# Performance work log

Measured on AMD Instinct MI355X. Metric: run time of the kernel, lower is better.

The kernel has to match this reference:

```python
import jax, jax.numpy as jnp
from jax import lax
import numpy as np

INPUT_DIM = 64
AUX_DIM = 32
HIDDEN = [512, 512]
OUTPUT_DIM = 128
BATCH = 64
SEQ = 512


def _lstm_params(key, in_dim, hidden):
    # PyTorch nn.LSTM init: U(-1/sqrt(H), 1/sqrt(H)); gate order i,f,g,o
    k = 1.0 / np.sqrt(hidden)
    ks = jax.random.split(key, 4)
    W_ih = jax.random.uniform(ks[0], (4 * hidden, in_dim), jnp.float32, -k, k)
    W_hh = jax.random.uniform(ks[1], (4 * hidden, hidden), jnp.float32, -k, k)
    b_ih = jax.random.uniform(ks[2], (4 * hidden,), jnp.float32, -k, k)
    b_hh = jax.random.uniform(ks[3], (4 * hidden,), jnp.float32, -k, k)
    return W_ih, W_hh, b_ih, b_hh


def setup_inputs() -> dict:
    key = jax.random.key(0)
    k_x, k_aux, k_l0, k_l1, k_w, k_b = jax.random.split(key, 6)
    primary_input = jax.random.normal(k_x, (BATCH, SEQ, INPUT_DIM), jnp.float32)
    auxiliary_input = jax.random.normal(k_aux, (BATCH, AUX_DIM), jnp.float32)
    W_ih0, W_hh0, b_ih0, b_hh0 = _lstm_params(k_l0, INPUT_DIM + AUX_DIM, HIDDEN[0])
    W_ih1, W_hh1, b_ih1, b_hh1 = _lstm_params(k_l1, HIDDEN[0], HIDDEN[1])
    k_out = 1.0 / np.sqrt(HIDDEN[-1])
    W_out = jax.random.uniform(k_w, (OUTPUT_DIM, HIDDEN[-1]), jnp.float32, -k_out, k_out)
    b_out = jax.random.uniform(k_b, (OUTPUT_DIM,), jnp.float32, -k_out, k_out)
    return {
        "primary_input": primary_input, "auxiliary_input": auxiliary_input,
        "W_ih0": W_ih0, "W_hh0": W_hh0, "b_ih0": b_ih0, "b_hh0": b_hh0,
        "W_ih1": W_ih1, "W_hh1": W_hh1, "b_ih1": b_ih1, "b_hh1": b_hh1,
        "W_out": W_out, "b_out": b_out,
    }


def _lstm_layer(x, W_ih, W_hh, b_ih, b_hh):
    # x: [B, S, D] -> hidden sequence [B, S, H]; zero initial (h, c)
    B = x.shape[0]
    H = W_hh.shape[1]
    # Precompute input projection for all timesteps: [B, S, 4H]
    x_proj = jnp.einsum('bsd,gd->bsg', x, W_ih) + b_ih + b_hh

    def step(carry, xt):
        h, c = carry  # [B, H] each
        gates = xt + h @ W_hh.T  # [B, 4H]
        i, f, g, o = jnp.split(gates, 4, axis=-1)
        i = jax.nn.sigmoid(i)
        f = jax.nn.sigmoid(f)
        g = jnp.tanh(g)
        o = jax.nn.sigmoid(o)
        c = f * c + i * g
        h = o * jnp.tanh(c)
        return (h, c), h

    h0 = jnp.zeros((B, H), x.dtype)
    (_, _), hs = lax.scan(step, (h0, h0), jnp.swapaxes(x_proj, 0, 1))
    return jnp.swapaxes(hs, 0, 1)  # [B, S, H]


def reference(primary_input, auxiliary_input,
              W_ih0, W_hh0, b_ih0, b_hh0,
              W_ih1, W_hh1, b_ih1, b_hh1,
              W_out, b_out):
    S = primary_input.shape[1]
    aux = jnp.broadcast_to(auxiliary_input[:, None, :],
                           (auxiliary_input.shape[0], S, auxiliary_input.shape[1]))
    x = jnp.concatenate([primary_input, aux], axis=2)  # [B, S, input+aux]
    x = _lstm_layer(x, W_ih0, W_hh0, b_ih0, b_hh0)
    x = _lstm_layer(x, W_ih1, W_hh1, b_ih1, b_hh1)
    last = x[:, -1, :]  # [B, H]
    return last @ W_out.T + b_out  # [B, output_dim]
```

## Files before the change

### kernel.cpp

```cpp
#include <hip/hip_runtime.h>

#define BATCH 64
#define SEQ   512
#define HID   512
#define DPRIM 64
#define DAUX  32
#define DIN   96
#define CT    16
#define NCHUNK 32
#define NBAT  32
#define WP    520
#define XPI   104
#define PST   33

#define WS_HB0HI  0u
#define WS_HB0LO  131072u
#define WS_HB1HI  262144u
#define WS_HB1LO  393216u
#define WS_SLOT0  524288u
#define WS_SLOT1  526336u
#define WS_GDONE  528384u
#define WS_XPD    530432u
#define WS_STATE_END 532480u
#define WS_PHH0HI 532480u
#define WS_PHH0LO 2629632u
#define WS_PHH1HI 4726784u
#define WS_PHH1LO 6823936u
#define WS_PIH1HI 8921088u
#define WS_PIH1LO 11018240u
#define WS_PIH0HI 13115392u
#define WS_PIH0LO 13508608u
#define WS_BSUM0  13901824u
#define WS_BSUM1  13910016u
#define WS_WOT    13918208u
#define WS_HIST   14180352u
#define WS_XP0    18374656u
#define WS_XP1    26763264u

typedef short s16x8 __attribute__((ext_vector_type(8)));
typedef float f32x4 __attribute__((ext_vector_type(4)));
typedef unsigned long long u64x2 __attribute__((ext_vector_type(2)));
typedef unsigned long long u64t;
typedef unsigned int u32t;
typedef unsigned short u16t;

__device__ __forceinline__ float sigm(float x)  { return 1.f / (1.f + __expf(-x)); }
__device__ __forceinline__ float tanh_f(float x){ return 1.f - 2.f / (__expf(2.f * x) + 1.f); }
__device__ __forceinline__ u16t f2b(float f) {
    u32t u = __float_as_uint(f);
    u += 0x7fffu + ((u >> 16) & 1u);
    return (u16t)(u >> 16);
}
__device__ __forceinline__ void split2(float f, u16t* hi, u16t* lo) {
    u16t h = f2b(f);
    float r = f - __uint_as_float((u32t)h << 16);
    *hi = h; *lo = f2b(r);
}
__device__ __forceinline__ u64t ld_coh64(const u64t* p) {
    return __hip_atomic_load(p, __ATOMIC_RELAXED, __HIP_MEMORY_SCOPE_AGENT);
}
__device__ __forceinline__ void st_coh64w(u64t* p, u64t v) {
    __hip_atomic_store(p, v, __ATOMIC_RELAXED, __HIP_MEMORY_SCOPE_AGENT);
}
__device__ __forceinline__ void st_cohf(float* p, float v) {
    __hip_atomic_store(p, v, __ATOMIC_RELAXED, __HIP_MEMORY_SCOPE_AGENT);
}
__device__ __forceinline__ int ld_slot(const int* p) {
    return __hip_atomic_load(p, __ATOMIC_RELAXED, __HIP_MEMORY_SCOPE_AGENT);
}
__device__ __forceinline__ void st_slot(int* p, int v) {
    __hip_atomic_store(p, v, __ATOMIC_RELAXED, __HIP_MEMORY_SCOPE_AGENT);
}
#define MFMA16(a,b,c) __builtin_amdgcn_mfma_f32_16x16x32_bf16(a,b,c,0,0,0)

__device__ __forceinline__ void load_afrag(const u16t* ph, const u16t* pl,
                                           int u0, int col, int kg, int rt, int kh,
                                           s16x8* ah, s16x8* al) {
    int r = rt * 16 + col;
    int grow = (r >> 3) * HID + u0 + (r & 7);
    const u16t* sh = ph + (size_t)grow * HID;
    const u16t* sl = pl + (size_t)grow * HID;
#pragma unroll
    for (int k2 = 0; k2 < 8; ++k2) {
        int ko = (kh * 8 + k2) * 32 + kg * 8;
        ah[k2] = *(const s16x8*)(sh + ko);
        al[k2] = *(const s16x8*)(sl + ko);
    }
}

__global__ void prep_kernel(const float* __restrict__ Wih0, const float* __restrict__ Whh0,
                            const float* __restrict__ bih0, const float* __restrict__ bhh0,
                            const float* __restrict__ Wih1, const float* __restrict__ Whh1,
                            const float* __restrict__ bih1, const float* __restrict__ bhh1,
                            const float* __restrict__ Wout, char* __restrict__ ws)
{
    int idx = blockIdx.x * 256 + threadIdx.x;
    u16t h, l;
    split2(Whh0[idx], &h, &l);
    ((u16t*)(ws + WS_PHH0HI))[idx] = h; ((u16t*)(ws + WS_PHH0LO))[idx] = l;
    split2(Whh1[idx], &h, &l);
    ((u16t*)(ws + WS_PHH1HI))[idx] = h; ((u16t*)(ws + WS_PHH1LO))[idx] = l;
    split2(Wih1[idx], &h, &l);
    ((u16t*)(ws + WS_PIH1HI))[idx] = h; ((u16t*)(ws + WS_PIH1LO))[idx] = l;
    if (idx < 2048 * 96) {
        split2(Wih0[idx], &h, &l);
        ((u16t*)(ws + WS_PIH0HI))[idx] = h; ((u16t*)(ws + WS_PIH0LO))[idx] = l;
    }
    if (idx < 2048) {
        ((float*)(ws + WS_BSUM0))[idx] = bih0[idx] + bhh0[idx];
        ((float*)(ws + WS_BSUM1))[idx] = bih1[idx] + bhh1[idx];
    }
    if (idx < 65536) {
        ((float*)(ws + WS_WOT))[idx] = Wout[(size_t)(idx & 127) * HID + (idx >> 7)];
    }
}

__device__ __forceinline__ void do_step(
    int t, int c, int tl, int tid, int col, int kg,
    int rt, int bt, int kh,
    int b0, int u0, int ug,
    const s16x8* ahf, const s16x8* alf,
    u16t* Hti, u16t* Htl, float* Ps, float* Cs,
    u16t* hbhi, u16t* hblo, int* slots_self,
    const float* xp_self, bool coh_xq, u32t* hist_ring)
{
    const int p = t & 1;
    float4 xq = {0.f, 0.f, 0.f, 0.f};
    if (tid < 256) {
        int b = tid >> 3, u = tid & 7;
        const float* xr = xp_self + (size_t)(b * CT + tl) * 32 + u * 4;
        if (coh_xq) {
            u64t w0 = ld_coh64((const u64t*)xr);
            u64t w1 = ld_coh64((const u64t*)xr + 1);
            xq.x = __uint_as_float((u32t)w0); xq.y = __uint_as_float((u32t)(w0 >> 32));
            xq.z = __uint_as_float((u32t)w1); xq.w = __uint_as_float((u32t)(w1 >> 32));
        } else {
            xq = *(const float4*)xr;
        }
    }
    if (tid < 64) {
        const int* sp = slots_self + tid * 4;
        while (true) {
            int v = ld_slot(sp);
            if (__all(v >= t)) break;
            __builtin_amdgcn_s_sleep(2);
        }
    }
    __syncthreads();
    asm volatile("" ::: "memory");
    {
        int bl  = tid & 31;
        int bk0 = tid >> 5;
        const u64t* gh = (const u64t*)hbhi;
        const u64t* gl = (const u64t*)hblo;
#pragma unroll
        for (int q = 0; q < 4; ++q) {
            int block = bk0 + q * 16;
            size_t tg = (((size_t)(p ^ 1) * 64 + block) * 64 + b0 + bl) * 2;
            u64t h0 = ld_coh64(gh + tg);
            u64t h1 = ld_coh64(gh + tg + 1);
            u64t l0 = ld_coh64(gl + tg);
            u64t l1 = ld_coh64(gl + tg + 1);
            int lt = (block * 32 + bl) * 8;
            *(u64x2*)(Hti + lt) = (u64x2){h0, h1};
            *(u64x2*)(Htl + lt) = (u64x2){l0, l1};
        }
    }
    __syncthreads();
    {
        f32x4 a0 = {0.f, 0.f, 0.f, 0.f}, a1 = {0.f, 0.f, 0.f, 0.f};
#pragma unroll
        for (int k2 = 0; k2 < 8; ++k2) {
            int blk = kh * 32 + k2 * 4 + kg;
            const u16t* hb = Hti + ((size_t)blk * 32 + bt * 16 + col) * 8;
            const u16t* lb = Htl + ((size_t)blk * 32 + bt * 16 + col) * 8;
            s16x8 bhv = *(const s16x8*)hb;
            s16x8 blv = *(const s16x8*)lb;
            a0 = MFMA16(ahf[k2], bhv, a0);
            a1 = MFMA16(ahf[k2], blv, a1);
            a0 = MFMA16(alf[k2], bhv, a0);
        }
        a0 = a0 + a1;
#pragma unroll
        for (int j = 0; j < 4; ++j)
            Ps[((kh << 5) + rt * 16 + kg * 4 + j) * PST + bt * 16 + col] = a0[j];
    }
    __syncthreads();
    if (tid < 256) {
        int b = tid >> 3, u = tid & 7;
        float gi = Ps[(u)      * PST + b] + Ps[(32 + u) * PST + b] + xq.x;
        float gf = Ps[(8 + u)  * PST + b] + Ps[(40 + u) * PST + b] + xq.y;
        float gg = Ps[(16 + u) * PST + b] + Ps[(48 + u) * PST + b] + xq.z;
        float go = Ps[(24 + u) * PST + b] + Ps[(56 + u) * PST + b] + xq.w;
        float si = sigm(gi), sf = sigm(gf), so = sigm(go);
        float tg = tanh_f(gg);
        float cN = sf * Cs[tid] + si * tg;
        Cs[tid] = cN;
        float hN = so * tanh_f(cN);
        u16t hi, lo; split2(hN, &hi, &lo);
        u32t wh = (u32t)hi | (((u32t)(u16t)__shfl_xor((int)hi, 1)) << 16);
        u32t wl = (u32t)lo | (((u32t)(u16t)__shfl_xor((int)lo, 1)) << 16);
        u64t qh = (u64t)wh | ((u64t)(u32t)__shfl_xor((int)wh, 2) << 32);
        u64t ql = (u64t)wl | ((u64t)(u32t)__shfl_xor((int)wl, 2) << 32);
        size_t tg2 = (((size_t)p * 64 + ug) * 64 + b0 + b) * 2;
        if ((u & 3) == 0) {
            st_coh64w((u64t*)hbhi + tg2 + (u >> 2), qh);
            st_coh64w((u64t*)hblo + tg2 + (u >> 2), ql);
        }
        if (hist_ring) {
            u32t pk = ((u32t)hi << 16) | (u32t)lo;
            u64t qp = (u64t)pk | ((u64t)(u32t)__shfl_xor((int)pk, 1) << 32);
            if ((u & 1) == 0)
                st_coh64w((u64t*)(hist_ring +
                    ((size_t)((c & 1) * BATCH + b0 + b) * CT + tl) * HID + u0 + u), qp);
        }
    }
    __syncthreads();
    if (tid == 0) st_slot(slots_self + ug * 4, t + 1);
}

__global__ __launch_bounds__(512, 2)
void mega_kernel(const float* __restrict__ prim, const float* __restrict__ aux,
                 char* __restrict__ ws)
{
    __shared__ __align__(16) unsigned char smem[156032];
    u16t* Hti  = (u16t*)smem;
    u16t* Htl  = (u16t*)(smem + 32768);
    u16t* Bthi = (u16t*)smem;
    u16t* Btlo = (u16t*)(smem + 66560);
    u16t* XWhi = (u16t*)(smem + 133120);
    u16t* XWlo = (u16t*)(smem + 139776);
    float* Ps  = (float*)(smem + 146432);
    float* Cs  = (float*)(smem + 154880);
    float* Bs  = (float*)(smem + 155904);

    const int tid  = threadIdx.x;
    const int wgid = blockIdx.x;
    const int layer = wgid >> 7;
    const int lwg  = wgid & 127;
    const int bg   = (lwg >> 2) & 1;
    const int ug   = ((lwg >> 3) << 2) | (lwg & 3);
    const int b0   = bg * NBAT;
    const int u0   = ug * 8;
    const int lane = tid & 63;
    const int wid  = tid >> 6;
    const int col  = lane & 15;
    const int kg   = lane >> 4;
    const int rt   = (wid >> 1) & 1;
    const int bt   = wid & 1;
    const int kh   = wid >> 2;

    u16t* hbhi = (u16t*)(ws + (layer ? WS_HB1HI : WS_HB0HI));
    u16t* hblo = (u16t*)(ws + (layer ? WS_HB1LO : WS_HB0LO));
    int* slots_self = (int*)(ws + (layer ? WS_SLOT1 : WS_SLOT0) + bg * 1024);
    int* slots_l0   = (int*)(ws + WS_SLOT0 + bg * 1024);
    int* gdone      = (int*)(ws + WS_GDONE + bg * 1024);
    int* xpd        = (int*)(ws + WS_XPD   + bg * 1024);
    const float* bsum = (const float*)(ws + (layer ? WS_BSUM1 : WS_BSUM0));
    u32t* hist = (u32t*)(ws + WS_HIST);
    float* xpregion = (float*)(ws + (layer ? WS_XP1 : WS_XP0));
    float* xp_self = xpregion + (size_t)lwg * 16384;

    if (tid < 256) Cs[tid] = 0.f;
    if (tid < 32) {
        int grow = (tid >> 3) * HID + u0 + (tid & 7);
        Bs[tid] = bsum[grow];
    }
    if (layer == 0) {
        for (int s = tid; s < 32 * 24; s += 512) {
            int rl = s / 24, sl = s % 24;
            int grow = (rl >> 3) * HID + u0 + (rl & 7);
            u64t v  = *((const u64t*)((u16t*)(ws + WS_PIH0HI) + (size_t)grow * DIN) + sl);
            u64t v2 = *((const u64t*)((u16t*)(ws + WS_PIH0LO) + (size_t)grow * DIN) + sl);
            *((u64t*)(XWhi + (size_t)rl * XPI) + sl) = v;
            *((u64t*)(XWlo + (size_t)rl * XPI) + sl) = v2;
        }
    }
    __syncthreads();

    if (layer == 0) {
        for (int c = 0; c < NCHUNK; ++c) {
            {
                f32x4 acc[4][2];
#pragma unroll
                for (int m4 = 0; m4 < 4; ++m4)
#pragma unroll
                    for (int nt = 0; nt < 2; ++nt)
                        acc[m4][nt] = (f32x4){0.f, 0.f, 0.f, 0.f};
#pragma unroll
                for (int kt = 0; kt < 3; ++kt) {
                    int k0 = kt * 32 + kg * 8;
                    s16x8 ah0 = *(const s16x8*)(XWhi + (size_t)(col) * XPI + k0);
                    s16x8 al0 = *(const s16x8*)(XWlo + (size_t)(col) * XPI + k0);
                    s16x8 ah1 = *(const s16x8*)(XWhi + (size_t)(16 + col) * XPI + k0);
                    s16x8 al1 = *(const s16x8*)(XWlo + (size_t)(16 + col) * XPI + k0);
#pragma unroll
                    for (int m4 = 0; m4 < 4; ++m4) {
                        int bb = wid * 4 + m4;
                        float xv[8];
                        if (kt < 2) {
                            const float* pr = prim + ((size_t)(b0 + bb) * SEQ + c * CT + col) * DPRIM + k0;
                            float4 v0 = *(const float4*)pr;
                            float4 v1 = *(const float4*)(pr + 4);
                            xv[0] = v0.x; xv[1] = v0.y; xv[2] = v0.z; xv[3] = v0.w;
                            xv[4] = v1.x; xv[5] = v1.y; xv[6] = v1.z; xv[7] = v1.w;
                        } else {
                            const float* ax = aux + (size_t)(b0 + bb) * DAUX + kg * 8;
                            float4 v0 = *(const float4*)ax;
                            float4 v1 = *(const float4*)(ax + 4);
                            xv[0] = v0.x; xv[1] = v0.y; xv[2] = v0.z; xv[3] = v0.w;
                            xv[4] = v1.x; xv[5] = v1.y; xv[6] = v1.z; xv[7] = v1.w;
                        }
                        u16t hh[8], ll[8];
#pragma unroll
                        for (int j = 0; j < 8; ++j) split2(xv[j], &hh[j], &ll[j]);
                        s16x8 bhv, blv;
#pragma unroll
                        for (int j = 0; j < 8; ++j) { bhv[j] = (short)hh[j]; blv[j] = (short)ll[j]; }
                        acc[m4][0] = MFMA16(ah0, bhv, acc[m4][0]);
                        acc[m4][0] = MFMA16(ah0, blv, acc[m4][0]);
                        acc[m4][0] = MFMA16(al0, bhv, acc[m4][0]);
                        acc[m4][1] = MFMA16(ah1, bhv, acc[m4][1]);
                        acc[m4][1] = MFMA16(ah1, blv, acc[m4][1]);
                        acc[m4][1] = MFMA16(al1, bhv, acc[m4][1]);
                    }
                }
#pragma unroll
                for (int m4 = 0; m4 < 4; ++m4) {
                    int m = (wid * 4 + m4) * 16 + col;
#pragma unroll
                    for (int nt = 0; nt < 2; ++nt)
#pragma unroll
                        for (int j = 0; j < 4; ++j) {
                            int gr = nt * 16 + kg * 4 + j;
                            xp_self[(size_t)m * 32 + (gr & 7) * 4 + (gr >> 3)] =
                                acc[m4][nt][j] + Bs[gr];
                        }
                }
            }
            s16x8 ahf[8], alf[8];
            load_afrag((const u16t*)(ws + WS_PHH0HI), (const u16t*)(ws + WS_PHH0LO),
                       u0, col, kg, rt, kh, ahf, alf);
            if (c >= 2) {
                if (tid < 64) {
                    while (true) {
                        int v = ld_slot(gdone + tid * 4);
                        if (__all(v >= c - 1)) break;
                        __builtin_amdgcn_s_sleep(2);
                    }
                }
            }
            __syncthreads();
            for (int tl = 0; tl < CT; ++tl)
                do_step(c * CT + tl, c, tl, tid, col, kg, rt, bt, kh, b0, u0, ug,
                        ahf, alf, Hti, Htl, Ps, Cs, hbhi, hblo, slots_self,
                        xp_self, false, hist);
        }
    } else {
        const int gm = ug >> 3, gn = ug & 7;
        for (int c = 0; c < NCHUNK; ++c) {
            if (tid < 64) {
                while (true) {
                    int v = ld_slot(slots_l0 + tid * 4);
                    if (__all(v >= (c + 1) * CT)) break;
                    __builtin_amdgcn_s_sleep(2);
                }
            }
            __syncthreads();
            {
                int i = tid >> 3, j = tid & 7;
                int m = gm * 64 + i;
                int gb = b0 + (m >> 4), tl2 = m & 15;
                const u64t* src = (const u64t*)(hist + ((size_t)((c & 1) * BATCH + gb) * CT + tl2) * HID);
                u64t* dh = (u64t*)(Bthi + (size_t)i * WP);
                u64t* dl = (u64t*)(Btlo + (size_t)i * WP);
#pragma unroll
                for (int q = 0; q < 16; ++q) {
                    int g = q * 8 + j;
                    u64t w0 = ld_coh64(src + g * 2);
                    u64t w1 = ld_coh64(src + g * 2 + 1);
                    u32t e0 = (u32t)w0, e1 = (u32t)(w0 >> 32);
                    u32t e2 = (u32t)w1, e3 = (u32t)(w1 >> 32);
                    dh[g] = (u64t)(e0 >> 16) | ((u64t)(e1 >> 16) << 16) |
                            ((u64t)(e2 >> 16) << 32) | ((u64t)(e3 >> 16) << 48);
                    dl[g] = (u64t)(e0 & 0xffffu) | ((u64t)(e1 & 0xffffu) << 16) |
                            ((u64t)(e2 & 0xffffu) << 32) | ((u64t)(e3 & 0xffffu) << 48);
                }
            }
            __syncthreads();
            if (tid == 0) st_slot(gdone + ug * 4, c + 1);
            {
                const u16t* pih = (const u16t*)(ws + WS_PIH1HI);
                const u16t* pil = (const u16t*)(ws + WS_PIH1LO);
                int Rb0 = gn * 256 + (wid * 2) * 16 + col;
                int Rb1 = Rb0 + 16;
                int g0 = ((Rb0 >> 3) & 3) * HID + (Rb0 >> 5) * 8 + (Rb0 & 7);
                int g1 = ((Rb1 >> 3) & 3) * HID + (Rb1 >> 5) * 8 + (Rb1 & 7);
                const u16t* a0h = pih + (size_t)g0 * HID;
                const u16t* a0l = pil + (size_t)g0 * HID;
                const u16t* a1h = pih + (size_t)g1 * HID;
                const u16t* a1l = pil + (size_t)g1 * HID;
                float biasv[2][4];
#pragma unroll
                for (int nt = 0; nt < 2; ++nt)
#pragma unroll
                    for (int j = 0; j < 4; ++j) {
                        int R = gn * 256 + (wid * 2 + nt) * 16 + kg * 4 + j;
                        biasv[nt][j] = bsum[((R >> 3) & 3) * HID + (R >> 5) * 8 + (R & 7)];
                    }
                f32x4 acc[4][2];
#pragma unroll
                for (int mt = 0; mt < 4; ++mt)
#pragma unroll
                    for (int nt = 0; nt < 2; ++nt)
                        acc[mt][nt] = (f32x4){0.f, 0.f, 0.f, 0.f};
                for (int kt = 0; kt < 16; ++kt) {
                    int k0 = kt * 32 + kg * 8;
                    s16x8 ah0 = *(const s16x8*)(a0h + k0), al0 = *(const s16x8*)(a0l + k0);
                    s16x8 ah1 = *(const s16x8*)(a1h + k0), al1 = *(const s16x8*)(a1l + k0);
#pragma unroll
                    for (int mt = 0; mt < 4; ++mt) {
                        const u16t* bth = Bthi + (size_t)(mt * 16 + col) * WP;
                        const u16t* btl = Btlo + (size_t)(mt * 16 + col) * WP;
                        s16x8 bhv = *(const s16x8*)(bth + k0), blv = *(const s16x8*)(btl + k0);
                        acc[mt][0] = MFMA16(ah0, bhv, acc[mt][0]);
                        acc[mt][0] = MFMA16(ah0, blv, acc[mt][0]);
                        acc[mt][0] = MFMA16(al0, bhv, acc[mt][0]);
                        acc[mt][1] = MFMA16(ah1, bhv, acc[mt][1]);
                        acc[mt][1] = MFMA16(ah1, blv, acc[mt][1]);
                        acc[mt][1] = MFMA16(al1, bhv, acc[mt][1]);
                    }
                }
#pragma unroll
                for (int mt = 0; mt < 4; ++mt)
#pragma unroll
                    for (int nt = 0; nt < 2; ++nt)
#pragma unroll
                        for (int j = 0; j < 4; ++j) {
                            int m = gm * 64 + mt * 16 + col;
                            int R = gn * 256 + (wid * 2 + nt) * 16 + kg * 4 + j;
                            int ugt = R >> 5, rl = R & 31;
                            int lwgt = ((ugt >> 2) << 3) | (bg << 2) | (ugt & 3);
                            st_cohf(xpregion + (size_t)lwgt * 16384 + (size_t)m * 32 +
                                        (rl & 7) * 4 + (rl >> 3),
                                    acc[mt][nt][j] + biasv[nt][j]);
                        }
            }
            __syncthreads();
            if (tid == 0) st_slot(xpd + ug * 4, c + 1);
            s16x8 ahf[8], alf[8];
            load_afrag((const u16t*)(ws + WS_PHH1HI), (const u16t*)(ws + WS_PHH1LO),
                       u0, col, kg, rt, kh, ahf, alf);
            if (tid < 64) {
                while (true) {
                    int v = ld_slot(xpd + tid * 4);
                    if (__all(v >= c + 1)) break;
                    __builtin_amdgcn_s_sleep(2);
                }
            }
            __syncthreads();
            for (int tl = 0; tl < CT; ++tl)
                do_step(c * CT + tl, c, tl, tid, col, kg, rt, bt, kh, b0, u0, ug,
                        ahf, alf, Hti, Htl, Ps, Cs, hbhi, hblo, slots_self,
                        xp_self, true, nullptr);
        }
    }
}

__global__ void outproj_kernel(const char* __restrict__ ws, const float* __restrict__ bout,
                               float* __restrict__ out)
{
    __shared__ float hs[HID];
    int b = blockIdx.x;
    const u16t* ph = (const u16t*)(ws + WS_HB1HI);
    const u16t* pl = (const u16t*)(ws + WS_HB1LO);
    for (int i = threadIdx.x; i < HID; i += 128) {
        size_t e = (((size_t)64 + (i >> 3)) * 64 + b) * 8 + (i & 7);
        hs[i] = __uint_as_float((u32t)ph[e] << 16) + __uint_as_float((u32t)pl[e] << 16);
    }
    __syncthreads();
    int o = threadIdx.x;
    const float* Wot = (const float*)(ws + WS_WOT);
    float acc = bout[o];
#pragma unroll 8
    for (int k = 0; k < HID; ++k) acc = fmaf(hs[k], Wot[k * 128 + o], acc);
    out[b * 128 + o] = acc;
}

extern "C" void kernel_launch(void* const* d_in, const int* in_sizes, int n_in,
                              void* d_out, int out_size, void* d_ws, size_t ws_size,
                              hipStream_t stream)
{
    (void)in_sizes; (void)n_in; (void)out_size; (void)ws_size;
    const float* prim = (const float*)d_in[0];
    const float* aux  = (const float*)d_in[1];
    const float* Wih0 = (const float*)d_in[2];
    const float* Whh0 = (const float*)d_in[3];
    const float* bih0 = (const float*)d_in[4];
    const float* bhh0 = (const float*)d_in[5];
    const float* Wih1 = (const float*)d_in[6];
    const float* Whh1 = (const float*)d_in[7];
    const float* bih1 = (const float*)d_in[8];
    const float* bhh1 = (const float*)d_in[9];
    const float* Wout = (const float*)d_in[10];
    const float* bout = (const float*)d_in[11];
    float* out = (float*)d_out;
    char* wsc  = (char*)d_ws;

    hipMemsetAsync(wsc, 0, WS_STATE_END, stream);
    prep_kernel<<<4096, 256, 0, stream>>>(Wih0, Whh0, bih0, bhh0,
                                          Wih1, Whh1, bih1, bhh1, Wout, wsc);

    void* margs[] = {(void*)&prim, (void*)&aux, (void*)&wsc};
    hipLaunchCooperativeKernel((void*)mega_kernel, dim3(256), dim3(512), margs, 0, stream);

    outproj_kernel<<<64, 128, 0, stream>>>(wsc, bout, out);
}
```

Measured before the change: 3.303 ms.

## Specialize warps per recurrent step to cut barriers and per-slot polling latency

Restructures the per-timestep recurrence so each of waves 0-6 polls only the producer slots for the h-blocks it loads, then gathers them immediately, instead of one wave polling all slots behind a block barrier. Gate math and cell state move to a single wave (wave 7) that keeps c in registers and packs outputs without shuffles. It then publishes with a vmcnt wait and a lane-0 slot store, which drops the trailing barrier of each step. This shortens the per-step critical path of the latency-bound recurrence. The trade-offs are fewer threads doing the elementwise work and a reliance on the next step's barrier for correct ordering of shared memory.

```diff
diff --git a/kernel.cpp b/kernel.cpp
--- a/kernel.cpp
+++ b/kernel.cpp
@@ -56,6 +56,9 @@
     float r = f - __uint_as_float((u32t)h << 16);
     *hi = h; *lo = f2b(r);
 }
+__device__ __forceinline__ u64t pack4(u16t a, u16t b, u16t c, u16t d) {
+    return (u64t)a | ((u64t)b << 16) | ((u64t)c << 32) | ((u64t)d << 48);
+}
 __device__ __forceinline__ u64t ld_coh64(const u64t* p) {
     return __hip_atomic_load(p, __ATOMIC_RELAXED, __HIP_MEMORY_SCOPE_AGENT);
 }
@@ -115,55 +118,60 @@
     }
 }
 
+template<bool ISL0>
 __device__ __forceinline__ void do_step(
-    int t, int c, int tl, int tid, int col, int kg,
+    int t, int c, int tl, int tid, int lane, int wid, int col, int kg,
     int rt, int bt, int kh,
     int b0, int u0, int ug,
     const s16x8* ahf, const s16x8* alf,
-    u16t* Hti, u16t* Htl, float* Ps, float* Cs,
+    u16t* Hti, u16t* Htl, float* Ps, float* cr,
     u16t* hbhi, u16t* hblo, int* slots_self,
-    const float* xp_self, bool coh_xq, u32t* hist_ring)
+    const float* xp_self, u32t* hist_ring)
 {
     const int p = t & 1;
-    float4 xq = {0.f, 0.f, 0.f, 0.f};
-    if (tid < 256) {
-        int b = tid >> 3, u = tid & 7;
-        const float* xr = xp_self + (size_t)(b * CT + tl) * 32 + u * 4;
-        if (coh_xq) {
-            u64t w0 = ld_coh64((const u64t*)xr);
-            u64t w1 = ld_coh64((const u64t*)xr + 1);
-            xq.x = __uint_as_float((u32t)w0); xq.y = __uint_as_float((u32t)(w0 >> 32));
-            xq.z = __uint_as_float((u32t)w1); xq.w = __uint_as_float((u32t)(w1 >> 32));
+    const int ab  = lane >> 1;
+    const int au4 = (lane & 1) * 4;
+    float xq[16];
+    if (wid == 7) {
+        const float* xr = xp_self + (size_t)(ab * CT + tl) * 32 + au4 * 4;
+        if (ISL0) {
+#pragma unroll
+            for (int q = 0; q < 4; ++q) {
+                float4 v = *(const float4*)(xr + q * 4);
+                xq[q*4+0]=v.x; xq[q*4+1]=v.y; xq[q*4+2]=v.z; xq[q*4+3]=v.w;
+            }
         } else {
-            xq = *(const float4*)xr;
-        }
-    }
-    if (tid < 64) {
-        const int* sp = slots_self + tid * 4;
-        while (true) {
-            int v = ld_slot(sp);
-            if (__all(v >= t)) break;
-            __builtin_amdgcn_s_sleep(2);
-        }
-    }
-    __syncthreads();
-    asm volatile("" ::: "memory");
+#pragma unroll
+            for (int q = 0; q < 8; ++q) {
+                u64t w = ld_coh64((const u64t*)xr + q);
+                xq[q*2]   = __uint_as_float((u32t)w);
+                xq[q*2+1] = __uint_as_float((u32t)(w >> 32));
+            }
+        }
+    }
     {
-        int bl  = tid & 31;
-        int bk0 = tid >> 5;
-        const u64t* gh = (const u64t*)hbhi;
-        const u64t* gl = (const u64t*)hblo;
-#pragma unroll
-        for (int q = 0; q < 4; ++q) {
-            int block = bk0 + q * 16;
-            size_t tg = (((size_t)(p ^ 1) * 64 + block) * 64 + b0 + bl) * 2;
-            u64t h0 = ld_coh64(gh + tg);
-            u64t h1 = ld_coh64(gh + tg + 1);
-            u64t l0 = ld_coh64(gl + tg);
-            u64t l1 = ld_coh64(gl + tg + 1);
-            int lt = (block * 32 + bl) * 8;
-            *(u64x2*)(Hti + lt) = (u64x2){h0, h1};
-            *(u64x2*)(Htl + lt) = (u64x2){l0, l1};
+        const int nblk = (wid < 6) ? 10 : (wid == 6) ? 4 : 0;
+        const int blk0 = (wid < 6) ? wid * 10 : 60;
+        if (nblk > 0) {
+            const int* sp = slots_self + (blk0 + (lane < nblk ? lane : 0)) * 4;
+            while (true) {
+                int v = ld_slot(sp);
+                if (__all(v >= t)) break;
+                __builtin_amdgcn_s_sleep(1);
+            }
+            asm volatile("" ::: "memory");
+            int half = lane >> 5, bat = lane & 31;
+            const u64t* gp = (const u64t*)(half ? hblo : hbhi);
+            u16t* lp = half ? Htl : Hti;
+#pragma unroll
+            for (int i = 0; i < 10; ++i) {
+                if (i >= nblk) break;
+                int blk = blk0 + i;
+                size_t g = (((size_t)(p ^ 1) * 64 + blk) * 64 + b0 + bat) * 2;
+                u64t v0 = ld_coh64(gp + g);
+                u64t v1 = ld_coh64(gp + g + 1);
+                *(u64x2*)(lp + ((size_t)blk * 32 + bat) * 8) = (u64x2){v0, v1};
+            }
         }
     }
     __syncthreads();
@@ -186,37 +194,40 @@
             Ps[((kh << 5) + rt * 16 + kg * 4 + j) * PST + bt * 16 + col] = a0[j];
     }
     __syncthreads();
-    if (tid < 256) {
-        int b = tid >> 3, u = tid & 7;
-        float gi = Ps[(u)      * PST + b] + Ps[(32 + u) * PST + b] + xq.x;
-        float gf = Ps[(8 + u)  * PST + b] + Ps[(40 + u) * PST + b] + xq.y;
-        float gg = Ps[(16 + u) * PST + b] + Ps[(48 + u) * PST + b] + xq.z;
-        float go = Ps[(24 + u) * PST + b] + Ps[(56 + u) * PST + b] + xq.w;
-        float si = sigm(gi), sf = sigm(gf), so = sigm(go);
-        float tg = tanh_f(gg);
-        float cN = sf * Cs[tid] + si * tg;
-        Cs[tid] = cN;
-        float hN = so * tanh_f(cN);
-        u16t hi, lo; split2(hN, &hi, &lo);
-        u32t wh = (u32t)hi | (((u32t)(u16t)__shfl_xor((int)hi, 1)) << 16);
-        u32t wl = (u32t)lo | (((u32t)(u16t)__shfl_xor((int)lo, 1)) << 16);
-        u64t qh = (u64t)wh | ((u64t)(u32t)__shfl_xor((int)wh, 2) << 32);
-        u64t ql = (u64t)wl | ((u64t)(u32t)__shfl_xor((int)wl, 2) << 32);
-        size_t tg2 = (((size_t)p * 64 + ug) * 64 + b0 + b) * 2;
-        if ((u & 3) == 0) {
-            st_coh64w((u64t*)hbhi + tg2 + (u >> 2), qh);
-            st_coh64w((u64t*)hblo + tg2 + (u >> 2), ql);
-        }
-        if (hist_ring) {
-            u32t pk = ((u32t)hi << 16) | (u32t)lo;
-            u64t qp = (u64t)pk | ((u64t)(u32t)__shfl_xor((int)pk, 1) << 32);
-            if ((u & 1) == 0)
-                st_coh64w((u64t*)(hist_ring +
-                    ((size_t)((c & 1) * BATCH + b0 + b) * CT + tl) * HID + u0 + u), qp);
-        }
-    }
-    __syncthreads();
-    if (tid == 0) st_slot(slots_self + ug * 4, t + 1);
+    if (wid == 7) {
+        u16t hhv[4], llv[4];
+        u32t pk[4];
+#pragma unroll
+        for (int k = 0; k < 4; ++k) {
+            int u = au4 + k;
+            float gi = Ps[(u)      * PST + ab] + Ps[(32 + u) * PST + ab] + xq[k*4+0];
+            float gf = Ps[(8 + u)  * PST + ab] + Ps[(40 + u) * PST + ab] + xq[k*4+1];
+            float gg = Ps[(16 + u) * PST + ab] + Ps[(48 + u) * PST + ab] + xq[k*4+2];
+            float go = Ps[(24 + u) * PST + ab] + Ps[(56 + u) * PST + ab] + xq[k*4+3];
+            float si = sigm(gi), sf = sigm(gf), so = sigm(go);
+            float tg = tanh_f(gg);
+            float cN = sf * cr[k] + si * tg;
+            cr[k] = cN;
+            float hN = so * tanh_f(cN);
+            split2(hN, &hhv[k], &llv[k]);
+            pk[k] = ((u32t)hhv[k] << 16) | (u32t)llv[k];
+        }
+        u64t qh = pack4(hhv[0], hhv[1], hhv[2], hhv[3]);
+        u64t ql = pack4(llv[0], llv[1], llv[2], llv[3]);
+        size_t e2 = (((size_t)p * 64 + ug) * 64 + b0 + ab) * 2 + (au4 >> 2);
+        st_coh64w((u64t*)hbhi + e2, qh);
+        st_coh64w((u64t*)hblo + e2, ql);
+        if (ISL0) {
+            u64t q0 = (u64t)pk[0] | ((u64t)pk[1] << 32);
+            u64t q1 = (u64t)pk[2] | ((u64t)pk[3] << 32);
+            u64t* hp = (u64t*)(hist_ring +
+                ((size_t)((c & 1) * BATCH + b0 + ab) * CT + tl) * HID + u0 + au4);
+            st_coh64w(hp, q0);
+            st_coh64w(hp + 1, q1);
+        }
+        asm volatile("s_waitcnt vmcnt(0)" ::: "memory");
+        if (lane == 0) st_slot(slots_self + ug * 4, t + 1);
+    }
 }
 
 __global__ __launch_bounds__(512, 2)
@@ -231,7 +242,6 @@
     u16t* XWhi = (u16t*)(smem + 133120);
     u16t* XWlo = (u16t*)(smem + 139776);
     float* Ps  = (float*)(smem + 146432);
-    float* Cs  = (float*)(smem + 154880);
     float* Bs  = (float*)(smem + 155904);
 
     const int tid  = threadIdx.x;
@@ -261,7 +271,8 @@
     float* xpregion = (float*)(ws + (layer ? WS_XP1 : WS_XP0));
     float* xp_self = xpregion + (size_t)lwg * 16384;
 
-    if (tid < 256) Cs[tid] = 0.f;
+    float cr[4] = {0.f, 0.f, 0.f, 0.f};
+
     if (tid < 32) {
         int grow = (tid >> 3) * HID + u0 + (tid & 7);
         Bs[tid] = bsum[grow];
@@ -352,9 +363,10 @@
             }
             __syncthreads();
             for (int tl = 0; tl < CT; ++tl)
-                do_step(c * CT + tl, c, tl, tid, col, kg, rt, bt, kh, b0, u0, ug,
-                        ahf, alf, Hti, Htl, Ps, Cs, hbhi, hblo, slots_self,
-                        xp_self, false, hist);
+                do_step<true>(c * CT + tl, c, tl, tid, lane, wid, col, kg, rt, bt, kh,
+                              b0, u0, ug, ahf, alf, Hti, Htl, Ps, cr,
+                              hbhi, hblo, slots_self, xp_self, hist);
+            __syncthreads();
         }
     } else {
         const int gm = ug >> 3, gn = ug & 7;
@@ -460,9 +472,10 @@
             }
             __syncthreads();
             for (int tl = 0; tl < CT; ++tl)
-                do_step(c * CT + tl, c, tl, tid, col, kg, rt, bt, kh, b0, u0, ug,
-                        ahf, alf, Hti, Htl, Ps, Cs, hbhi, hblo, slots_self,
-                        xp_self, true, nullptr);
+                do_step<false>(c * CT + tl, c, tl, tid, lane, wid, col, kg, rt, bt, kh,
+                               b0, u0, ug, ahf, alf, Hti, Htl, Ps, cr,
+                               hbhi, hblo, slots_self, xp_self, nullptr);
+            __syncthreads();
         }
     }
 }
```

New measurement: 4.753 ms. +43.9%, slower.

## Replace per-workgroup step barriers with per-wavefront fine-grained slot flags

Applied to the files above, without the earlier changes.

Changes the recurrent step synchronisation so that each wavefront waits only on the slots of the producer blocks whose hidden-state data it loads, and each wavefront publishes its own slot after its stores drain. This removes the two workgroup-wide __syncthreads and the all-wave flag poll per timestep. The slot array grows to one entry per wave per producer, and do_step is templated on the layer. The layer-1 chunk wait now polls all 256 slots. The risk is memory-ordering subtlety, since correctness now depends on s_waitcnt and on coherent loads rather than on barriers.

```diff
diff --git a/kernel.cpp b/kernel.cpp
--- a/kernel.cpp
+++ b/kernel.cpp
@@ -18,24 +18,24 @@
 #define WS_HB1HI  262144u
 #define WS_HB1LO  393216u
 #define WS_SLOT0  524288u
-#define WS_SLOT1  526336u
-#define WS_GDONE  528384u
-#define WS_XPD    530432u
-#define WS_STATE_END 532480u
-#define WS_PHH0HI 532480u
-#define WS_PHH0LO 2629632u
-#define WS_PHH1HI 4726784u
-#define WS_PHH1LO 6823936u
-#define WS_PIH1HI 8921088u
-#define WS_PIH1LO 11018240u
-#define WS_PIH0HI 13115392u
-#define WS_PIH0LO 13508608u
-#define WS_BSUM0  13901824u
-#define WS_BSUM1  13910016u
-#define WS_WOT    13918208u
-#define WS_HIST   14180352u
-#define WS_XP0    18374656u
-#define WS_XP1    26763264u
+#define WS_SLOT1  532480u
+#define WS_GDONE  540672u
+#define WS_XPD    542720u
+#define WS_STATE_END 544768u
+#define WS_PHH0HI 544768u
+#define WS_PHH0LO 2641920u
+#define WS_PHH1HI 4739072u
+#define WS_PHH1LO 6836224u
+#define WS_PIH1HI 8933376u
+#define WS_PIH1LO 11030528u
+#define WS_PIH0HI 13127680u
+#define WS_PIH0LO 13520896u
+#define WS_BSUM0  13914112u
+#define WS_BSUM1  13922304u
+#define WS_WOT    13930496u
+#define WS_HIST   14192640u
+#define WS_XP0    18386944u
+#define WS_XP1    26775552u
 
 typedef short s16x8 __attribute__((ext_vector_type(8)));
 typedef float f32x4 __attribute__((ext_vector_type(4)));
@@ -115,38 +115,37 @@
     }
 }
 
+template<bool ISL0>
 __device__ __forceinline__ void do_step(
-    int t, int c, int tl, int tid, int col, int kg,
+    int t, int c, int tl, int tid, int lane, int wid, int col, int kg,
     int rt, int bt, int kh,
     int b0, int u0, int ug,
     const s16x8* ahf, const s16x8* alf,
     u16t* Hti, u16t* Htl, float* Ps, float* Cs,
     u16t* hbhi, u16t* hblo, int* slots_self,
-    const float* xp_self, bool coh_xq, u32t* hist_ring)
+    const float* xp_self, u32t* hist_ring)
 {
     const int p = t & 1;
     float4 xq = {0.f, 0.f, 0.f, 0.f};
     if (tid < 256) {
         int b = tid >> 3, u = tid & 7;
         const float* xr = xp_self + (size_t)(b * CT + tl) * 32 + u * 4;
-        if (coh_xq) {
+        if (ISL0) {
+            xq = *(const float4*)xr;
+        } else {
             u64t w0 = ld_coh64((const u64t*)xr);
             u64t w1 = ld_coh64((const u64t*)xr + 1);
             xq.x = __uint_as_float((u32t)w0); xq.y = __uint_as_float((u32t)(w0 >> 32));
             xq.z = __uint_as_float((u32t)w1); xq.w = __uint_as_float((u32t)(w1 >> 32));
-        } else {
-            xq = *(const float4*)xr;
-        }
-    }
-    if (tid < 64) {
-        const int* sp = slots_self + tid * 4;
-        while (true) {
-            int v = ld_slot(sp);
-            if (__all(v >= t)) break;
-            __builtin_amdgcn_s_sleep(2);
-        }
-    }
-    __syncthreads();
+        }
+    }
+    if (lane < 32) {
+        int aw  = lane >> 3;
+        int bi  = lane & 7;
+        int blk = 2 * wid + (bi & 1) + 16 * (bi >> 1);
+        const int* sp = slots_self + (aw * 64 + blk) * 4;
+        while (ld_slot(sp) < t) __builtin_amdgcn_s_sleep(1);
+    }
     asm volatile("" ::: "memory");
     {
         int bl  = tid & 31;
@@ -207,16 +206,16 @@
             st_coh64w((u64t*)hbhi + tg2 + (u >> 2), qh);
             st_coh64w((u64t*)hblo + tg2 + (u >> 2), ql);
         }
-        if (hist_ring) {
+        if (ISL0) {
             u32t pk = ((u32t)hi << 16) | (u32t)lo;
             u64t qp = (u64t)pk | ((u64t)(u32t)__shfl_xor((int)pk, 1) << 32);
             if ((u & 1) == 0)
                 st_coh64w((u64t*)(hist_ring +
                     ((size_t)((c & 1) * BATCH + b0 + b) * CT + tl) * HID + u0 + u), qp);
         }
-    }
-    __syncthreads();
-    if (tid == 0) st_slot(slots_self + ug * 4, t + 1);
+        asm volatile("s_waitcnt vmcnt(0)" ::: "memory");
+        if (lane == 0) st_slot(slots_self + (wid * 64 + ug) * 4, t + 1);
+    }
 }
 
 __global__ __launch_bounds__(512, 2)
@@ -252,8 +251,8 @@
 
     u16t* hbhi = (u16t*)(ws + (layer ? WS_HB1HI : WS_HB0HI));
     u16t* hblo = (u16t*)(ws + (layer ? WS_HB1LO : WS_HB0LO));
-    int* slots_self = (int*)(ws + (layer ? WS_SLOT1 : WS_SLOT0) + bg * 1024);
-    int* slots_l0   = (int*)(ws + WS_SLOT0 + bg * 1024);
+    int* slots_self = (int*)(ws + (layer ? WS_SLOT1 : WS_SLOT0) + bg * 4096);
+    int* slots_l0   = (int*)(ws + WS_SLOT0 + bg * 4096);
     int* gdone      = (int*)(ws + WS_GDONE + bg * 1024);
     int* xpd        = (int*)(ws + WS_XPD   + bg * 1024);
     const float* bsum = (const float*)(ws + (layer ? WS_BSUM1 : WS_BSUM0));
@@ -352,19 +351,16 @@
             }
             __syncthreads();
             for (int tl = 0; tl < CT; ++tl)
-                do_step(c * CT + tl, c, tl, tid, col, kg, rt, bt, kh, b0, u0, ug,
-                        ahf, alf, Hti, Htl, Ps, Cs, hbhi, hblo, slots_self,
-                        xp_self, false, hist);
+                do_step<true>(c * CT + tl, c, tl, tid, lane, wid, col, kg, rt, bt, kh,
+                              b0, u0, ug, ahf, alf, Hti, Htl, Ps, Cs,
+                              hbhi, hblo, slots_self, xp_self, hist);
         }
     } else {
         const int gm = ug >> 3, gn = ug & 7;
         for (int c = 0; c < NCHUNK; ++c) {
-            if (tid < 64) {
-                while (true) {
-                    int v = ld_slot(slots_l0 + tid * 4);
-                    if (__all(v >= (c + 1) * CT)) break;
-                    __builtin_amdgcn_s_sleep(2);
-                }
+            if (tid < 256) {
+                const int* sp = slots_l0 + tid * 4;
+                while (ld_slot(sp) < (c + 1) * CT) __builtin_amdgcn_s_sleep(2);
             }
             __syncthreads();
             {
@@ -460,9 +456,9 @@
             }
             __syncthreads();
             for (int tl = 0; tl < CT; ++tl)
-                do_step(c * CT + tl, c, tl, tid, col, kg, rt, bt, kh, b0, u0, ug,
-                        ahf, alf, Hti, Htl, Ps, Cs, hbhi, hblo, slots_self,
-                        xp_self, true, nullptr);
+                do_step<false>(c * CT + tl, c, tl, tid, lane, wid, col, kg, rt, bt, kh,
+                               b0, u0, ug, ahf, alf, Hti, Htl, Ps, Cs,
+                               hbhi, hblo, slots_self, xp_self, nullptr);
         }
     }
 }
```

Measured after the change: 3.990 ms. +20.8%, slower.
